# Performance work log

Measured on AMD Instinct MI355X. Metric: run time of the kernel, lower is better.

## Reference

```python
import jax, jax.numpy as jnp
import numpy as np

N, E, NNZ, F = 65536, 16384, 786432, 128
ALPHA, BETA = 0.5, 0.5


def _linear(x, w, b):
    # torch nn.Linear: x @ W^T + b, W is [out,in]
    return x @ w.T + b


def _spmm_to_edges(vals, node_idx, hedge_idx, m):
    # (sparse [E,N]) @ m[N,F] -> [E,F]
    return jax.ops.segment_sum(vals[:, None] * m[node_idx], hedge_idx, num_segments=E)


def _spmm_to_nodes(vals, node_idx, hedge_idx, m):
    # (sparse [N,E]) @ m[E,F] -> [N,F]
    return jax.ops.segment_sum(vals[:, None] * m[hedge_idx], node_idx, num_segments=N)


def setup_inputs() -> dict:
    key = jax.random.key(0)
    ks = jax.random.split(key, 16)
    stdv = 1.0 / np.sqrt(F)
    u = lambda k, shp: jax.random.uniform(k, shp, jnp.float32, -stdv, stdv)
    return {
        "x": jax.random.normal(ks[0], (N, F), jnp.float32),
        "y": jax.random.normal(ks[1], (E, F), jnp.float32),
        "node_idx": jax.random.randint(ks[2], (NNZ,), 0, N, jnp.int32),
        "hedge_idx": jax.random.randint(ks[3], (NNZ,), 0, E, jnp.int32),
        "hd_vals": jax.random.uniform(ks[4], (NNZ,), jnp.float32),
        "hb_vals": jax.random.uniform(ks[5], (NNZ,), jnp.float32),
        "dhwd_vals": jax.random.uniform(ks[6], (NNZ,), jnp.float32),
        "bhub_vals": jax.random.uniform(ks[7], (NNZ,), jnp.float32),
        "Qv_w": u(ks[8], (F, F)), "Qv_b": u(ks[9], (F,)),
        "Qe_w": u(ks[10], (F, F)), "Qe_b": u(ks[11], (F,)),
        "Pe_w": u(ks[12], (F, F)), "Pe_b": u(ks[13], (F,)),
        "Pv_w": u(ks[14], (F, F)), "Pv_b": u(ks[15], (F,)),
    }


def reference(x, y, node_idx, hedge_idx, hd_vals, hb_vals, dhwd_vals, bhub_vals,
              Qv_w, Qv_b, Qe_w, Qe_b, Pe_w, Pe_b, Pv_w, Pv_b):
    qvx = _linear(x, Qv_w, Qv_b)          # [N,F]
    qey = _linear(y, Qe_w, Qe_b)          # [E,F]
    pey = _linear(y, Pe_w, Pe_b)          # [E,F]
    pvx = _linear(x, Pv_w, Pv_b)          # [N,F]
    # X = DHWD @ (alpha * (HD @ Qv(x)) + (1-alpha) * Qe(y))
    t_e = ALPHA * _spmm_to_edges(hd_vals, node_idx, hedge_idx, qvx) + (1.0 - ALPHA) * qey
    X = _spmm_to_nodes(dhwd_vals, node_idx, hedge_idx, t_e)
    # Y = BHUB @ (beta * (HB @ Pe(y)) + (1-beta) * Pv(x))
    t_n = BETA * _spmm_to_nodes(hb_vals, node_idx, hedge_idx, pey) + (1.0 - BETA) * pvx
    Y = _spmm_to_edges(bhub_vals, node_idx, hedge_idx, t_n)
    return (X, Y)
```

## Files before the change

### kernel.cpp

```cpp
#include <hip/hip_runtime.h>

#define F 128
#define NN 65536
#define EE 16384
#define NNZT 786432

typedef __attribute__((ext_vector_type(8))) short bfrag8;
typedef __attribute__((ext_vector_type(4))) float f32x4;

__device__ __forceinline__ unsigned int bfrn(float f) {
    unsigned int u = __float_as_uint(f);
    return (u + 0x7fffu + ((u >> 16) & 1u)) >> 16;
}

__global__ void hist_kernel(const int4* __restrict__ hedge_idx4,
                            const int4* __restrict__ node_idx4,
                            int* __restrict__ cnt_e, int* __restrict__ cnt_n) {
    int i = blockIdx.x * 256 + threadIdx.x;
    int4 e = hedge_idx4[i];
    int4 n = node_idx4[i];
    atomicAdd(&cnt_e[e.x], 1);
    atomicAdd(&cnt_e[e.y], 1);
    atomicAdd(&cnt_e[e.z], 1);
    atomicAdd(&cnt_e[e.w], 1);
    atomicAdd(&cnt_n[n.x], 1);
    atomicAdd(&cnt_n[n.y], 1);
    atomicAdd(&cnt_n[n.z], 1);
    atomicAdd(&cnt_n[n.w], 1);
}

__global__ __launch_bounds__(1024) void scan_p1(const int* __restrict__ cnt,
                                                int* __restrict__ ofs,
                                                int* __restrict__ bsum) {
    __shared__ int wsum[16];
    int t = threadIdx.x, lane = t & 63, w = t >> 6;
    int g = blockIdx.x * 1024 + t;
    int v = cnt[g];
    int inc = v;
#pragma unroll
    for (int d = 1; d < 64; d <<= 1) {
        int u = __shfl_up(inc, d);
        if (lane >= d) inc += u;
    }
    if (lane == 63) wsum[w] = inc;
    __syncthreads();
    if (t < 16) {
        int s = wsum[t];
#pragma unroll
        for (int d = 1; d < 16; d <<= 1) {
            int u = __shfl_up(s, d);
            if (t >= d) s += u;
        }
        wsum[t] = s;
    }
    __syncthreads();
    int woff = (w == 0) ? 0 : wsum[w - 1];
    ofs[g] = woff + inc - v;
    if (t == 1023) bsum[blockIdx.x] = wsum[15];
}

__global__ void scan_p2(int* __restrict__ bsum, int nb, int* __restrict__ ofs_end) {
    int lane = threadIdx.x;
    int v = (lane < nb) ? bsum[lane] : 0;
    int inc = v;
#pragma unroll
    for (int d = 1; d < 64; d <<= 1) {
        int u = __shfl_up(inc, d);
        if (lane >= d) inc += u;
    }
    if (lane < nb) bsum[lane] = inc - v;
    if (lane == 63) *ofs_end = inc;
}

__global__ __launch_bounds__(1024) void scan_p3(int* __restrict__ ofs,
                                                const int* __restrict__ bsum) {
    int g = blockIdx.x * 1024 + threadIdx.x;
    ofs[g] += bsum[blockIdx.x];
}

__global__ void invfill_kernel(const int* __restrict__ node_idx, const int* __restrict__ hedge_idx,
                               const int* __restrict__ ofs_e, const int* __restrict__ ofs_n,
                               int* __restrict__ cur_e, int* __restrict__ cur_n,
                               int* __restrict__ inv_e, int* __restrict__ inv_n) {
    int i = blockIdx.x * 256 + threadIdx.x;
    int e = hedge_idx[i];
    int pe = atomicAdd(&cur_e[e], 1);
    inv_e[ofs_e[e] + pe] = i;
    int n = node_idx[i];
    int pn = atomicAdd(&cur_n[n], 1);
    inv_n[ofs_n[n] + pn] = i;
}

__global__ void wprep_kernel(const float* __restrict__ W0, const float* __restrict__ W1,
                             const float* __restrict__ W2, const float* __restrict__ W3,
                             unsigned short* __restrict__ whi, unsigned short* __restrict__ wlo) {
    int mat = blockIdx.x >> 6;
    int off = (blockIdx.x & 63) * 256 + threadIdx.x;
    const float* W = (mat == 0) ? W0 : (mat == 1) ? W1 : (mat == 2) ? W2 : W3;
    float f = W[off];
    unsigned int h = bfrn(f);
    float hf = __uint_as_float(h << 16);
    unsigned int l = bfrn(f - hf);
    int idx = mat * 16384 + off;
    whi[idx] = (unsigned short)h;
    wlo[idx] = (unsigned short)l;
}

template <bool ABF16, bool BBF16>
__global__ __launch_bounds__(256, 2) void gemm_mfma(const float* __restrict__ in,
                                                    const unsigned short* __restrict__ whi,
                                                    const unsigned short* __restrict__ wlo,
                                                    const float* __restrict__ bA,
                                                    const float* __restrict__ bB,
                                                    void* __restrict__ outA,
                                                    void* __restrict__ outB) {
    __shared__ uint4 AH[2][4][64];
    __shared__ uint4 AL[2][4][64];
    int t = threadIdx.x;
    int wv = t >> 6, lane = t & 63;
    int row0 = blockIdx.x * 128;

    int mat = wv >> 1;
    const unsigned short* wh = whi + mat * 16384;
    const unsigned short* wl = wlo + mat * 16384;
    int colbase = (wv & 1) * 64;
    int ln15 = lane & 15;
    int kb = 8 * (lane >> 4);

    bfrag8 bh[4][4], bl[4][4];
#pragma unroll
    for (int ct = 0; ct < 4; ++ct) {
        int n = colbase + ct * 16 + ln15;
#pragma unroll
        for (int ks = 0; ks < 4; ++ks) {
            bh[ct][ks] = *(const bfrag8*)&wh[n * 128 + ks * 32 + kb];
            bl[ct][ks] = *(const bfrag8*)&wl[n * 128 + ks * 32 + kb];
        }
    }
    const float* bias = mat ? bB : bA;
    float biasv[4];
#pragma unroll
    for (int ct = 0; ct < 4; ++ct) biasv[ct] = bias[colbase + ct * 16 + ln15];
    void* outp = mat ? outB : outA;
    bool obf = mat ? BBF16 : ABF16;

    auto STAGE = [&](int rt, int b) {
        int r = row0 + rt * 16 + ln15;
        int k0 = wv * 32 + kb;
        const float* p = &in[(size_t)r * 128 + k0];
        float4 f0 = *(const float4*)p;
        float4 f1 = *(const float4*)(p + 4);
        float fs[8] = {f0.x, f0.y, f0.z, f0.w, f1.x, f1.y, f1.z, f1.w};
        unsigned int hi[4], lo[4];
#pragma unroll
        for (int q = 0; q < 4; ++q) {
            unsigned int h0 = bfrn(fs[2 * q]);
            unsigned int h1 = bfrn(fs[2 * q + 1]);
            float hf0 = __uint_as_float(h0 << 16);
            float hf1 = __uint_as_float(h1 << 16);
            unsigned int l0 = bfrn(fs[2 * q] - hf0);
            unsigned int l1 = bfrn(fs[2 * q + 1] - hf1);
            hi[q] = h0 | (h1 << 16);
            lo[q] = l0 | (l1 << 16);
        }
        AH[b][wv][lane] = make_uint4(hi[0], hi[1], hi[2], hi[3]);
        AL[b][wv][lane] = make_uint4(lo[0], lo[1], lo[2], lo[3]);
    };

    STAGE(0, 0);
    __syncthreads();
    for (int rt = 0; rt < 8; ++rt) {
        int b = rt & 1;
        if (rt < 7) STAGE(rt + 1, b ^ 1);
        f32x4 acc[4];
#pragma unroll
        for (int ct = 0; ct < 4; ++ct) acc[ct] = (f32x4){0.f, 0.f, 0.f, 0.f};
#pragma unroll
        for (int ks = 0; ks < 4; ++ks) {
            bfrag8 ah = *(const bfrag8*)&AH[b][ks][lane];
            bfrag8 al = *(const bfrag8*)&AL[b][ks][lane];
#pragma unroll
            for (int ct = 0; ct < 4; ++ct)
                acc[ct] = __builtin_amdgcn_mfma_f32_16x16x32_bf16(ah, bh[ct][ks], acc[ct], 0, 0, 0);
#pragma unroll
            for (int ct = 0; ct < 4; ++ct)
                acc[ct] = __builtin_amdgcn_mfma_f32_16x16x32_bf16(ah, bl[ct][ks], acc[ct], 0, 0, 0);
#pragma unroll
            for (int ct = 0; ct < 4; ++ct)
                acc[ct] = __builtin_amdgcn_mfma_f32_16x16x32_bf16(al, bh[ct][ks], acc[ct], 0, 0, 0);
        }
        int rbase = row0 + rt * 16 + (lane >> 4) * 4;
#pragma unroll
        for (int ct = 0; ct < 4; ++ct) {
            int c = colbase + ct * 16 + ln15;
#pragma unroll
            for (int rg = 0; rg < 4; ++rg) {
                float v = acc[ct][rg] + biasv[ct];
                if (obf)
                    ((unsigned short*)outp)[(size_t)(rbase + rg) * 128 + c] = (unsigned short)bfrn(v);
                else
                    ((float*)outp)[(size_t)(rbase + rg) * 128 + c] = v;
            }
        }
        __syncthreads();
    }
}

template <int U, bool BF16OUT, bool HASINIT>
__global__ __launch_bounds__(256) void spmm_g(const int* __restrict__ ofs,
                                              const int* __restrict__ inv,
                                              const int* __restrict__ idxarr,
                                              const float* __restrict__ valarr,
                                              float vscale,
                                              const unsigned short* __restrict__ src,
                                              const float* __restrict__ initsrc,
                                              float iscale,
                                              void* __restrict__ outp) {
    int row = blockIdx.x * 4 + (threadIdx.x >> 6);
    int lane = threadIdx.x & 63;
    int q = lane >> 4;
    int li = lane & 15;
    int o0 = ofs[row], o1 = ofs[row + 1];
    float acc[8] = {};
    for (int j = o0; j < o1; j += 4 * U) {
#pragma unroll
        for (int u = 0; u < U; ++u) {
            int slot = j + 4 * u + q;
            bool ok = slot < o1;
            int ss = ok ? slot : o0;
            int iv = inv[ss];
            int tg = idxarr[iv];
            float v = ok ? valarr[iv] * vscale : 0.f;
            uint4 rb = *(const uint4*)&src[(size_t)tg * F + li * 8];
            unsigned int rw0 = rb.x, rw1 = rb.y, rw2 = rb.z, rw3 = rb.w;
            acc[0] += v * __uint_as_float(rw0 << 16);
            acc[1] += v * __uint_as_float(rw0 & 0xffff0000u);
            acc[2] += v * __uint_as_float(rw1 << 16);
            acc[3] += v * __uint_as_float(rw1 & 0xffff0000u);
            acc[4] += v * __uint_as_float(rw2 << 16);
            acc[5] += v * __uint_as_float(rw2 & 0xffff0000u);
            acc[6] += v * __uint_as_float(rw3 << 16);
            acc[7] += v * __uint_as_float(rw3 & 0xffff0000u);
        }
    }
#pragma unroll
    for (int k = 0; k < 8; ++k) {
        acc[k] += __shfl_down(acc[k], 32);
        acc[k] += __shfl_down(acc[k], 16);
    }
    if (q == 0) {
        if (HASINIT) {
            const float4* ip = (const float4*)&initsrc[(size_t)row * F + li * 8];
            float4 i0 = ip[0], i1 = ip[1];
            acc[0] += iscale * i0.x;
            acc[1] += iscale * i0.y;
            acc[2] += iscale * i0.z;
            acc[3] += iscale * i0.w;
            acc[4] += iscale * i1.x;
            acc[5] += iscale * i1.y;
            acc[6] += iscale * i1.z;
            acc[7] += iscale * i1.w;
        }
        if (BF16OUT) {
            unsigned short* ob = (unsigned short*)outp;
            uint4 wv;
            wv.x = bfrn(acc[0]) | (bfrn(acc[1]) << 16);
            wv.y = bfrn(acc[2]) | (bfrn(acc[3]) << 16);
            wv.z = bfrn(acc[4]) | (bfrn(acc[5]) << 16);
            wv.w = bfrn(acc[6]) | (bfrn(acc[7]) << 16);
            *(uint4*)&ob[(size_t)row * F + li * 8] = wv;
        } else {
            float* of = (float*)outp;
            float4 s0 = {acc[0], acc[1], acc[2], acc[3]};
            float4 s1 = {acc[4], acc[5], acc[6], acc[7]};
            *(float4*)&of[(size_t)row * F + li * 8] = s0;
            *(float4*)&of[(size_t)row * F + li * 8 + 4] = s1;
        }
    }
}

extern "C" void kernel_launch(void* const* d_in, const int* in_sizes, int n_in,
                              void* d_out, int out_size, void* d_ws, size_t ws_size,
                              hipStream_t stream) {
    const float* x = (const float*)d_in[0];
    const float* y = (const float*)d_in[1];
    const int* node_idx = (const int*)d_in[2];
    const int* hedge_idx = (const int*)d_in[3];
    const float* hd_vals = (const float*)d_in[4];
    const float* hb_vals = (const float*)d_in[5];
    const float* dhwd_vals = (const float*)d_in[6];
    const float* bhub_vals = (const float*)d_in[7];
    const float* Qv_w = (const float*)d_in[8];
    const float* Qv_b = (const float*)d_in[9];
    const float* Qe_w = (const float*)d_in[10];
    const float* Qe_b = (const float*)d_in[11];
    const float* Pe_w = (const float*)d_in[12];
    const float* Pe_b = (const float*)d_in[13];
    const float* Pv_w = (const float*)d_in[14];
    const float* Pv_b = (const float*)d_in[15];

    float* X = (float*)d_out;
    float* Y = (float*)d_out + (size_t)NN * F;
    float* pvx = X;
    float* qey = Y;

    char* w = (char*)d_ws;
    unsigned short* qvx_b = (unsigned short*)(w + 0);
    unsigned short* pey_b = (unsigned short*)(w + 16777216);
    unsigned short* t_e_b = (unsigned short*)(w + 20971520);
    unsigned short* t_n_b = (unsigned short*)(w + 25165824);
    int* inv_e = (int*)(w + 41943040);
    int* inv_n = (int*)(w + 45088768);
    int* cnt_e = (int*)(w + 48234496);
    int* cnt_n = (int*)(w + 48300032);
    int* cur_e = (int*)(w + 48562176);
    int* cur_n = (int*)(w + 48627712);
    int* ofs_e = (int*)(w + 48889856);
    int* ofs_n = (int*)(w + 48956416);
    int* bsum  = (int*)(w + 49219072);
    unsigned short* whi = (unsigned short*)(w + 49219328);
    unsigned short* wlo = (unsigned short*)(w + 49350400);

    (void)hipMemsetAsync(cnt_e, 0, (size_t)2 * (EE + NN) * 4, stream);

    hist_kernel<<<NNZT / 1024, 256, 0, stream>>>((const int4*)hedge_idx, (const int4*)node_idx,
                                                 cnt_e, cnt_n);

    scan_p1<<<EE / 1024, 1024, 0, stream>>>(cnt_e, ofs_e, bsum);
    scan_p2<<<1, 64, 0, stream>>>(bsum, EE / 1024, &ofs_e[EE]);
    scan_p3<<<EE / 1024, 1024, 0, stream>>>(ofs_e, bsum);
    scan_p1<<<NN / 1024, 1024, 0, stream>>>(cnt_n, ofs_n, bsum);
    scan_p2<<<1, 64, 0, stream>>>(bsum, NN / 1024, &ofs_n[NN]);
    scan_p3<<<NN / 1024, 1024, 0, stream>>>(ofs_n, bsum);

    invfill_kernel<<<NNZT / 256, 256, 0, stream>>>(node_idx, hedge_idx, ofs_e, ofs_n,
                                                   cur_e, cur_n, inv_e, inv_n);

    wprep_kernel<<<256, 256, 0, stream>>>(Qv_w, Pv_w, Qe_w, Pe_w, whi, wlo);

    gemm_mfma<true, false><<<NN / 128, 256, 0, stream>>>(x, whi, wlo, Qv_b, Pv_b, qvx_b, pvx);
    gemm_mfma<false, true><<<EE / 128, 256, 0, stream>>>(y, whi + 2 * 16384, wlo + 2 * 16384,
                                                         Qe_b, Pe_b, qey, pey_b);

    spmm_g<4, true, true><<<EE / 4, 256, 0, stream>>>(ofs_e, inv_e, node_idx, hd_vals, 0.5f,
                                                      qvx_b, qey, 0.5f, t_e_b);
    spmm_g<2, true, true><<<NN / 4, 256, 0, stream>>>(ofs_n, inv_n, hedge_idx, hb_vals, 0.5f,
                                                      pey_b, pvx, 0.5f, t_n_b);

    spmm_g<2, false, false><<<NN / 4, 256, 0, stream>>>(ofs_n, inv_n, hedge_idx, dhwd_vals, 1.0f,
                                                        t_e_b, nullptr, 0.f, X);
    spmm_g<4, false, false><<<EE / 4, 256, 0, stream>>>(ofs_e, inv_e, node_idx, bhub_vals, 1.0f,
                                                        t_n_b, nullptr, 0.f, Y);
}
```

Baseline: 515.6 us.

## Slice inverse-index fill by destination range so each block group scatters locally

Replaces the one-thread-per-nonzero inverse fill with a sliced kernel. Each block handles one of eight index ranges, reads all indices with int4 loads, and only does atomics and scatter writes for entries whose hyperedge or node falls in its range. This keeps the atomic counters and inverse-array writes for a slice within a smaller address window, aiming for better L2/cache locality. In exchange every block group rereads the whole index arrays, eight times the index traffic.

```diff
diff --git a/kernel.cpp b/kernel.cpp
--- a/kernel.cpp
+++ b/kernel.cpp
@@ -78,17 +78,38 @@
     ofs[g] += bsum[blockIdx.x];
 }
 
-__global__ void invfill_kernel(const int* __restrict__ node_idx, const int* __restrict__ hedge_idx,
-                               const int* __restrict__ ofs_e, const int* __restrict__ ofs_n,
-                               int* __restrict__ cur_e, int* __restrict__ cur_n,
-                               int* __restrict__ inv_e, int* __restrict__ inv_n) {
-    int i = blockIdx.x * 256 + threadIdx.x;
-    int e = hedge_idx[i];
-    int pe = atomicAdd(&cur_e[e], 1);
-    inv_e[ofs_e[e] + pe] = i;
-    int n = node_idx[i];
-    int pn = atomicAdd(&cur_n[n], 1);
-    inv_n[ofs_n[n] + pn] = i;
+__global__ __launch_bounds__(256) void invfill_sliced(const int4* __restrict__ hedge4,
+                                                      const int4* __restrict__ node4,
+                                                      const int* __restrict__ ofs_e,
+                                                      const int* __restrict__ ofs_n,
+                                                      int* __restrict__ cur_e,
+                                                      int* __restrict__ cur_n,
+                                                      int* __restrict__ inv_e,
+                                                      int* __restrict__ inv_n) {
+    int slice = blockIdx.x & 7;
+    int bs = blockIdx.x >> 3;
+    int elo = slice << 11, ehi = elo + (EE >> 3);
+    int nlo = slice << 13, nhi = nlo + (NN >> 3);
+    for (int i4 = bs * 256 + threadIdx.x; i4 < NNZT / 4; i4 += 96 * 256) {
+        int4 e4 = hedge4[i4];
+        int4 n4 = node4[i4];
+        int base = i4 * 4;
+        int es[4] = {e4.x, e4.y, e4.z, e4.w};
+        int ns[4] = {n4.x, n4.y, n4.z, n4.w};
+#pragma unroll
+        for (int u = 0; u < 4; ++u) {
+            int e = es[u];
+            if (e >= elo && e < ehi) {
+                int p = atomicAdd(&cur_e[e], 1);
+                inv_e[ofs_e[e] + p] = base + u;
+            }
+            int n = ns[u];
+            if (n >= nlo && n < nhi) {
+                int p = atomicAdd(&cur_n[n], 1);
+                inv_n[ofs_n[n] + p] = base + u;
+            }
+        }
+    }
 }
 
 __global__ void wprep_kernel(const float* __restrict__ W0, const float* __restrict__ W1,
@@ -333,8 +354,8 @@
     scan_p2<<<1, 64, 0, stream>>>(bsum, NN / 1024, &ofs_n[NN]);
     scan_p3<<<NN / 1024, 1024, 0, stream>>>(ofs_n, bsum);
 
-    invfill_kernel<<<NNZT / 256, 256, 0, stream>>>(node_idx, hedge_idx, ofs_e, ofs_n,
-                                                   cur_e, cur_n, inv_e, inv_n);
+    invfill_sliced<<<768, 256, 0, stream>>>((const int4*)hedge_idx, (const int4*)node_idx,
+                                            ofs_e, ofs_n, cur_e, cur_n, inv_e, inv_n);
 
     wprep_kernel<<<256, 256, 0, stream>>>(Qv_w, Pv_w, Qe_w, Pe_w, whi, wlo);
 
```

After: 499.1 us. 1.03x faster.
